# Performance work log

Hardware: AMD Instinct MI355X
Metric: run time of the kernel (lower is better)

## Reference

```python
import jax, jax.numpy as jnp
import numpy as np

B, S, D, H = 2, 2048, 1024, 16  # batch, seq_len, model dim, heads


def setup_inputs() -> dict:
    key = jax.random.key(0)
    ks = jax.random.split(key, 5)
    return {
        "x": jax.random.normal(ks[0], (B, S, D), jnp.float32),
        "idx": jax.random.randint(ks[1], (B,), 0, S),
        "weight": jnp.float32(0.5),
        "attn_forcing": 1,  # static python flag
        "w_qkv": jax.random.normal(ks[2], (D, 3 * D), jnp.float32) * 0.02,
        "b_qkv": jnp.zeros((3 * D,), jnp.float32),
        "w_proj": jax.random.normal(ks[3], (D, D), jnp.float32) * 0.02,
        "b_proj": jnp.zeros((D,), jnp.float32),
    }


def reference(x, idx, weight, attn_forcing, w_qkv, b_qkv, w_proj, b_proj):
    Bx, Sx, Dm = x.shape
    dh = Dm // H
    # qkv projection (Conv1D: x @ w + b)
    qkv = x @ w_qkv + b_qkv  # [B,S,3D]
    q, k, v = jnp.split(qkv, 3, axis=-1)
    q = q.reshape(Bx, Sx, H, dh).transpose(0, 2, 1, 3)  # [B,H,S,dh]
    k = k.reshape(Bx, Sx, H, dh).transpose(0, 2, 1, 3)
    v = v.reshape(Bx, Sx, H, dh).transpose(0, 2, 1, 3)
    alen = jnp.arange(Sx)
    mask = (alen[None, :] <= alen[:, None]).astype(x.dtype)  # [S,S] causal
    w = jnp.einsum('bhqd,bhkd->bhqk', q, k) / jnp.asarray(np.sqrt(dh), x.dtype)
    w = w * mask + jnp.asarray(-1e9, x.dtype) * (1 - mask)
    w = jax.nn.softmax(w, axis=-1)
    if attn_forcing:
        # post-softmax forcing reweight: positions >= idx scaled by weight, then renorm
        a = jnp.where(alen[None, :] >= idx[:, None], weight, jnp.asarray(1.0, x.dtype))  # [B,S]
        w = w * a[:, None, None, :]
        w = w / jnp.sum(w, axis=-1, keepdims=True)
    out = jnp.einsum('bhqk,bhkd->bhqd', w, v)  # [B,H,S,dh]
    out = out.transpose(0, 2, 1, 3).reshape(Bx, Sx, Dm)  # merge heads
    return out @ w_proj + b_proj
```

## Files before the change

### kernel.cpp

```cpp
#include <hip/hip_runtime.h>


typedef __attribute__((ext_vector_type(8))) short short8;
typedef __attribute__((ext_vector_type(4))) float f32x4;

#define MFMA_B16(a, b, c) __builtin_amdgcn_mfma_f32_16x16x32_bf16(a, b, c, 0, 0, 0)

#if __has_builtin(__builtin_amdgcn_exp2f)
#define EXP2(x) __builtin_amdgcn_exp2f(x)
#else
#define EXP2(x) exp2f(x)
#endif

static __device__ __forceinline__ unsigned short f2bf(float f) {
    union { float f; unsigned int u; } v;
    v.f = f;
    unsigned int r = (v.u + 0x7fffu + ((v.u >> 16) & 1u)) >> 16;
    return (unsigned short)r;
}

static __device__ __forceinline__ unsigned int pk_bf16(float a, float b) {
#if __has_builtin(__builtin_amdgcn_cvt_pk_bf16_f32)
    typedef __bf16 bf2 __attribute__((ext_vector_type(2)));
    union { bf2 v; unsigned int u; } c;
    c.v = __builtin_amdgcn_cvt_pk_bf16_f32(a, b);
    return c.u;
#else
    return (unsigned int)f2bf(a) | ((unsigned int)f2bf(b) << 16);
#endif
}

static __device__ __forceinline__ void gl_lds16(const void* g, void* l) {
    __builtin_amdgcn_global_load_lds(
        (const __attribute__((address_space(1))) unsigned int*)g,
        (__attribute__((address_space(3))) unsigned int*)l, 16, 0, 0);
}

__global__ __launch_bounds__(256) void prep_kernel(const float4* __restrict__ x,
                                                   ushort4* __restrict__ xb,
                                                   const float* __restrict__ wqkv,
                                                   unsigned short* __restrict__ wqkvT,
                                                   const float* __restrict__ wproj,
                                                   unsigned short* __restrict__ wprojT) {
    const int bid = blockIdx.x;
    if (bid < 4096) {
        int i = bid * 256 + threadIdx.x;
        float4 v = x[i];
        ushort4 o;
        o.x = f2bf(v.x); o.y = f2bf(v.y); o.z = f2bf(v.z); o.w = f2bf(v.w);
        xb[i] = o;
        return;
    }
    __shared__ float t[32][33];
    const float* in;
    unsigned short* out;
    int R, C, bx, by;
    if (bid < 4096 + 3072) {
        int g = bid - 4096;
        in = wqkv; out = wqkvT; R = 1024; C = 3072;
        bx = g % 96; by = g / 96;
    } else {
        int g = bid - 7168;
        in = wproj; out = wprojT; R = 1024; C = 1024;
        bx = g & 31; by = g >> 5;
    }
    const int c0 = bx * 32, r0 = by * 32;
    const int xx = threadIdx.x & 31, yy0 = threadIdx.x >> 5;
    #pragma unroll
    for (int yy = yy0; yy < 32; yy += 8)
        t[yy][xx] = in[(size_t)(r0 + yy) * C + (c0 + xx)];
    __syncthreads();
    #pragma unroll
    for (int yy = yy0; yy < 32; yy += 8)
        out[(size_t)(c0 + yy) * R + (r0 + xx)] = f2bf(t[xx][yy]);
}

__global__ __launch_bounds__(256) void gemm_qkv_kernel(const unsigned short* __restrict__ A,
                                                       const unsigned short* __restrict__ Bt,
                                                       const float* __restrict__ bias,
                                                       unsigned short* __restrict__ q,
                                                       unsigned short* __restrict__ k,
                                                       unsigned short* __restrict__ vT) {
    __shared__ unsigned short As[128 * 64];
    __shared__ unsigned short Bs[128 * 64];
    const int tid = threadIdx.x;
    const int lane = tid & 63, wave = tid >> 6;
    const int l15 = lane & 15, quad = lane >> 4;
    const int wm = wave >> 1, wn = wave & 1;
    const int row0 = blockIdx.y * 128, col0 = blockIdx.x * 128;
    const int K = 1024;
    const bool isV = (blockIdx.x >= 16);

    int srow[4], scol[4], sdst[4];
    #pragma unroll
    for (int h = 0; h < 4; ++h) {
        int D = h * 256 + wave * 64 + lane;
        srow[h] = D >> 3;
        scol[h] = ((D & 7) ^ (srow[h] & 7)) * 8;
        sdst[h] = (h * 256 + wave * 64) * 8;
    }

    f32x4 acc[4][4] = {};

    for (int kt = 0; kt < K; kt += 64) {
        #pragma unroll
        for (int h = 0; h < 4; ++h) {
            gl_lds16(&A[(size_t)(row0 + srow[h]) * K + kt + scol[h]], &As[sdst[h]]);
            gl_lds16(&Bt[(size_t)(col0 + srow[h]) * K + kt + scol[h]], &Bs[sdst[h]]);
        }
        __syncthreads();
        #pragma unroll
        for (int kk = 0; kk < 2; ++kk) {
            short8 af[4], bf[4];
            #pragma unroll
            for (int i = 0; i < 4; ++i) {
                int r = wm * 64 + i * 16 + l15;
                af[i] = *(const short8*)&As[r * 64 + (((kk * 4 + quad) ^ (r & 7)) * 8)];
            }
            #pragma unroll
            for (int j = 0; j < 4; ++j) {
                int r = wn * 64 + j * 16 + l15;
                bf[j] = *(const short8*)&Bs[r * 64 + (((kk * 4 + quad) ^ (r & 7)) * 8)];
            }
            if (isV) {
                #pragma unroll
                for (int i = 0; i < 4; ++i)
                    #pragma unroll
                    for (int j = 0; j < 4; ++j)
                        acc[i][j] = MFMA_B16(af[i], bf[j], acc[i][j]);
            } else {
                #pragma unroll
                for (int i = 0; i < 4; ++i)
                    #pragma unroll
                    for (int j = 0; j < 4; ++j)
                        acc[i][j] = MFMA_B16(bf[j], af[i], acc[i][j]);
            }
        }
        __syncthreads();
    }

    const int b = row0 >> 11;
    const int s0 = row0 & 2047;
    const float* bb = bias + col0 + wn * 64;

    if (!isV) {
        const int which = blockIdx.x >> 3;
        unsigned short* dst = which ? k : q;
        const float scale = which ? 1.0f : 0.1803368867f;
        const int hh = ((blockIdx.x & 7) << 1) + wn;
        #pragma unroll
        for (int i = 0; i < 4; ++i) {
            const int s = s0 + wm * 64 + i * 16 + l15;
            unsigned short* drow = dst + ((size_t)((b * 16 + hh) * 2048 + s)) * 64;
            #pragma unroll
            for (int j = 0; j < 4; ++j) {
                float4 b4 = ((const float4*)bb)[j * 4 + quad];
                uint2 pv;
                pv.x = pk_bf16((acc[i][j][0] + b4.x) * scale, (acc[i][j][1] + b4.y) * scale);
                pv.y = pk_bf16((acc[i][j][2] + b4.z) * scale, (acc[i][j][3] + b4.w) * scale);
                *(uint2*)&drow[j * 16 + quad * 4] = pv;
            }
        }
    } else {
        const int hh = ((blockIdx.x - 16) << 1) + wn;
        #pragma unroll
        for (int j = 0; j < 4; ++j) {
            const int d = j * 16 + l15;
            const float bv = bb[d];
            unsigned short* drow = vT + ((size_t)((b * 16 + hh) * 64 + d)) * 2048 + s0;
            #pragma unroll
            for (int i = 0; i < 4; ++i) {
                uint2 pv;
                pv.x = pk_bf16(acc[i][j][0] + bv, acc[i][j][1] + bv);
                pv.y = pk_bf16(acc[i][j][2] + bv, acc[i][j][3] + bv);
                *(uint2*)&drow[wm * 64 + i * 16 + quad * 4] = pv;
            }
        }
    }
}

__global__ __launch_bounds__(256) void gemm_proj_kernel(const unsigned short* __restrict__ A,
                                                        const unsigned short* __restrict__ Bt,
                                                        const float* __restrict__ bias,
                                                        float* __restrict__ out) {
    __shared__ unsigned short As[128 * 64];
    __shared__ unsigned short Bs[64 * 64];
    const int tid = threadIdx.x;
    const int lane = tid & 63, wave = tid >> 6;
    const int l15 = lane & 15, quad = lane >> 4;
    const int wm = wave >> 1, wn = wave & 1;
    const int row0 = blockIdx.y * 128, col0 = blockIdx.x * 64;
    const int K = 1024;

    int srow[4], scol[4], sdst[4];
    #pragma unroll
    for (int h = 0; h < 4; ++h) {
        int D = h * 256 + wave * 64 + lane;
        srow[h] = D >> 3;
        scol[h] = ((D & 7) ^ (srow[h] & 7)) * 8;
        sdst[h] = (h * 256 + wave * 64) * 8;
    }

    f32x4 acc[4][2] = {};

    for (int kt = 0; kt < K; kt += 64) {
        #pragma unroll
        for (int h = 0; h < 4; ++h)
            gl_lds16(&A[(size_t)(row0 + srow[h]) * K + kt + scol[h]], &As[sdst[h]]);
        #pragma unroll
        for (int h = 0; h < 2; ++h)
            gl_lds16(&Bt[(size_t)(col0 + srow[h]) * K + kt + scol[h]], &Bs[sdst[h]]);
        __syncthreads();
        #pragma unroll
        for (int kk = 0; kk < 2; ++kk) {
            short8 af[4], bf[2];
            #pragma unroll
            for (int i = 0; i < 4; ++i) {
                int r = wm * 64 + i * 16 + l15;
                af[i] = *(const short8*)&As[r * 64 + (((kk * 4 + quad) ^ (r & 7)) * 8)];
            }
            #pragma unroll
            for (int j = 0; j < 2; ++j) {
                int r = wn * 32 + j * 16 + l15;
                bf[j] = *(const short8*)&Bs[r * 64 + (((kk * 4 + quad) ^ (r & 7)) * 8)];
            }
            #pragma unroll
            for (int i = 0; i < 4; ++i)
                #pragma unroll
                for (int j = 0; j < 2; ++j)
                    acc[i][j] = MFMA_B16(bf[j], af[i], acc[i][j]);
        }
        __syncthreads();
    }

    const float* bb = bias + col0 + wn * 32;
    #pragma unroll
    for (int i = 0; i < 4; ++i) {
        const int row = row0 + wm * 64 + i * 16 + l15;
        #pragma unroll
        for (int j = 0; j < 2; ++j) {
            float4 b4 = ((const float4*)bb)[j * 4 + quad];
            float4 ov;
            ov.x = acc[i][j][0] + b4.x;
            ov.y = acc[i][j][1] + b4.y;
            ov.z = acc[i][j][2] + b4.z;
            ov.w = acc[i][j][3] + b4.w;
            *(float4*)&out[(size_t)row * 1024 + col0 + wn * 32 + j * 16 + quad * 4] = ov;
        }
    }
}

__global__ __launch_bounds__(256) void attn_kernel(const unsigned short* __restrict__ Q,
                                                   const unsigned short* __restrict__ Kg,
                                                   const unsigned short* __restrict__ Vt,
                                                   const int* __restrict__ idx,
                                                   const float* __restrict__ weight,
                                                   const int* __restrict__ forcing,
                                                   unsigned short* __restrict__ O) {
    __shared__ unsigned short Ks[2][4096];
    __shared__ unsigned short Vs[2][4096];
    __shared__ unsigned short Pw[4][1024];

    const int tid = threadIdx.x;
    const int lane = tid & 63, wave = tid >> 6;
    const int l15 = lane & 15, quad = lane >> 4;
    const int bid = blockIdx.x;
    const int u = bid >> 5, a = u & 7, qg = u >> 3;
    const int t = (qg == 0) ? (31 - a) : (qg == 1) ? (16 + a) : (qg == 2) ? (15 - a) : a;
    const int bh = bid & 31;
    const int b = bh >> 4, hh = bh & 15;
    const unsigned short* Qb = Q + (size_t)bh * 2048 * 64;
    const unsigned short* Kh = Kg + (size_t)bh * 2048 * 64;
    const unsigned short* Vh = Vt + (size_t)bh * 2048 * 64;

    const int idxb = idx[b];
    const float lw = (forcing[0] != 0) ? __log2f(weight[0]) : 0.0f;

    const int L0 = wave * 128 + lane;
    const int rS = L0 >> 3;
    const int cS = (L0 & 7) ^ (rS & 7);
    const int ldsOffJ0 = (wave * 128) * 8;
    const int ldsOffJ1 = (wave * 128 + 64) * 8;

    const int q0 = t * 64 + wave * 16;
    const int qrow = q0 + l15;

    short8 aq0 = *(const short8*)&Qb[(q0 + l15) * 64 + quad * 8];
    short8 aq1 = *(const short8*)&Qb[(q0 + l15) * 64 + 32 + quad * 8];

    const short8 ones8 = {0x3F80, 0x3F80, 0x3F80, 0x3F80, 0x3F80, 0x3F80, 0x3F80, 0x3F80};

    f32x4 o[4] = {};
    f32x4 lsum = {};

    const int nkb = t + 1;

    {
        const unsigned short* kg = Kh + (size_t)rS * 64 + cS * 8;
        const unsigned short* vg = Vh + (size_t)rS * 2048 + cS * 8;
        gl_lds16(kg,            &Ks[0][ldsOffJ0]);
        gl_lds16(kg + 8 * 64,   &Ks[0][ldsOffJ1]);
        gl_lds16(vg,            &Vs[0][ldsOffJ0]);
        gl_lds16(vg + 8 * 2048, &Vs[0][ldsOffJ1]);
    }
    __syncthreads();

    unsigned short* const pwb = &Pw[wave][0];
    const int pwr = l15 * 64;
    const int pa7 = l15 & 7;

    for (int kb = 0; kb < nkb; ++kb) {
        const int cur = kb & 1;
        const int kbase = kb * 64;
        if (kb + 1 < nkb) {
            const int nb = kbase + 64;
            const unsigned short* kg = Kh + (size_t)(nb + rS) * 64 + cS * 8;
            const unsigned short* vg = Vh + (size_t)rS * 2048 + nb + cS * 8;
            gl_lds16(kg,            &Ks[cur ^ 1][ldsOffJ0]);
            gl_lds16(kg + 8 * 64,   &Ks[cur ^ 1][ldsOffJ1]);
            gl_lds16(vg,            &Vs[cur ^ 1][ldsOffJ0]);
            gl_lds16(vg + 8 * 2048, &Vs[cur ^ 1][ldsOffJ1]);
        }

        const bool fullF = (kbase >= idxb);
        const bool bndF = (!fullF) && (kbase + 63 >= idxb);
        const float zu = fullF ? lw : 0.0f;

        f32x4 sT[4];
        #pragma unroll
        for (int kt = 0; kt < 4; ++kt) {
            const int row = kt * 16 + l15;
            short8 k0 = *(const short8*)&Ks[cur][row * 64 + ((quad ^ (row & 7)) * 8)];
            short8 k1 = *(const short8*)&Ks[cur][row * 64 + (((4 + quad) ^ (row & 7)) * 8)];
            f32x4 z;
            if (!bndF) {
                z[0] = zu; z[1] = zu; z[2] = zu; z[3] = zu;
            } else {
                #pragma unroll
                for (int r = 0; r < 4; ++r)
                    z[r] = (kbase + kt * 16 + quad * 4 + r >= idxb) ? lw : 0.0f;
            }
            z = MFMA_B16(k0, aq0, z);
            z = MFMA_B16(k1, aq1, z);
            sT[kt] = z;
        }

        if (kb == t) {
            #pragma unroll
            for (int kt = 0; kt < 4; ++kt)
                #pragma unroll
                for (int r = 0; r < 4; ++r)
                    if (kbase + kt * 16 + quad * 4 + r > qrow) sT[kt][r] = -3.0e38f;
        }

        #pragma unroll
        for (int kt = 0; kt < 4; ++kt)
            #pragma unroll
            for (int r = 0; r < 4; ++r)
                sT[kt][r] = EXP2(sT[kt][r]);

        #pragma unroll
        for (int kt = 0; kt < 4; ++kt) {
            unsigned int* pw = (unsigned int*)&pwb[pwr +
                (((kt * 2 + (quad >> 1)) ^ pa7) * 8) + (quad & 1) * 4];
            pw[0] = pk_bf16(sT[kt][0], sT[kt][1]);
            pw[1] = pk_bf16(sT[kt][2], sT[kt][3]);
        }

        short8 bp0 = *(const short8*)&pwb[pwr + ((quad ^ pa7) * 8)];
        short8 bp1 = *(const short8*)&pwb[pwr + (((4 + quad) ^ pa7) * 8)];

        lsum = MFMA_B16(ones8, bp0, lsum);
        lsum = MFMA_B16(ones8, bp1, lsum);

        #pragma unroll
        for (int dt = 0; dt < 4; ++dt) {
            const int row = dt * 16 + l15;
            short8 vf0 = *(const short8*)&Vs[cur][row * 64 + ((quad ^ (row & 7)) * 8)];
            short8 vf1 = *(const short8*)&Vs[cur][row * 64 + (((4 + quad) ^ (row & 7)) * 8)];
            f32x4 oo = o[dt];
            oo = MFMA_B16(vf0, bp0, oo);
            oo = MFMA_B16(vf1, bp1, oo);
            o[dt] = oo;
        }

        __syncthreads();
    }

    const float inv = 1.0f / lsum[0];
    unsigned short* sc = &Ks[0][0] + wave * 1152;
    #pragma unroll
    for (int dt = 0; dt < 4; ++dt)
        #pragma unroll
        for (int r = 0; r < 4; ++r)
            sc[l15 * 72 + dt * 16 + quad * 4 + r] = f2bf(o[dt][r] * inv);
    const size_t rowoff = ((size_t)(b * 2048 + q0 + l15)) * 1024 + hh * 64;
    #pragma unroll
    for (int h = 0; h < 2; ++h) {
        short8 v8 = *(const short8*)&sc[l15 * 72 + quad * 16 + h * 8];
        *(short8*)&O[rowoff + quad * 16 + h * 8] = v8;
    }
}

extern "C" void kernel_launch(void* const* d_in, const int* in_sizes, int n_in,
                              void* d_out, int out_size, void* d_ws, size_t ws_size,
                              hipStream_t stream) {
    const float* x        = (const float*)d_in[0];
    const int*   idx      = (const int*)d_in[1];
    const float* weight   = (const float*)d_in[2];
    const int*   forcing  = (const int*)d_in[3];
    const float* w_qkv    = (const float*)d_in[4];
    const float* b_qkv    = (const float*)d_in[5];
    const float* w_proj   = (const float*)d_in[6];
    const float* b_proj   = (const float*)d_in[7];
    float* out = (float*)d_out;

    char* ws = (char*)d_ws;
    unsigned short* xb      = (unsigned short*)(ws);
    unsigned short* wqkvT   = (unsigned short*)(ws + 8388608);
    unsigned short* wprojT  = (unsigned short*)(ws + 14680064);
    unsigned short* qbuf    = (unsigned short*)(ws + 16777216);
    unsigned short* kbuf    = (unsigned short*)(ws + 25165824);
    unsigned short* vTbuf   = (unsigned short*)(ws + 33554432);
    unsigned short* attn_out = xb;

    prep_kernel<<<8192, 256, 0, stream>>>((const float4*)x, (ushort4*)xb,
                                          w_qkv, wqkvT, w_proj, wprojT);
    gemm_qkv_kernel<<<dim3(24, 32), 256, 0, stream>>>(xb, wqkvT, b_qkv, qbuf, kbuf, vTbuf);
    attn_kernel<<<1024, 256, 0, stream>>>(qbuf, kbuf, vTbuf, idx, weight, forcing, attn_out);
    gemm_proj_kernel<<<dim3(16, 32), 256, 0, stream>>>(attn_out, wprojT, b_proj, out);
}
```

Baseline: 189.4 us.

## Process two query tiles per attention block to reuse staged K/V

Each attention workgroup now handles 128 query rows (two 64-row tiles, A and B) instead of 64. Every K/V tile loaded into LDS therefore feeds both tiles, roughly halving global K/V traffic and the number of blocks launched. Tile A skips its last key block on the diagonal. The grid shrinks from 1024 to 512 blocks, the balanced t-ordering is replaced by a simple descending order, and register and LDS use per block increase. This risks lower occupancy and worse load balance across CUs.

```diff
diff --git a/kernel.cpp b/kernel.cpp
--- a/kernel.cpp
+++ b/kernel.cpp
@@ -259,14 +259,13 @@
                                                    unsigned short* __restrict__ O) {
     __shared__ unsigned short Ks[2][4096];
     __shared__ unsigned short Vs[2][4096];
-    __shared__ unsigned short Pw[4][1024];
+    __shared__ unsigned short Pw[4][2048];
 
     const int tid = threadIdx.x;
     const int lane = tid & 63, wave = tid >> 6;
     const int l15 = lane & 15, quad = lane >> 4;
     const int bid = blockIdx.x;
-    const int u = bid >> 5, a = u & 7, qg = u >> 3;
-    const int t = (qg == 0) ? (31 - a) : (qg == 1) ? (16 + a) : (qg == 2) ? (15 - a) : a;
+    const int t = 15 - (bid >> 5);
     const int bh = bid & 31;
     const int b = bh >> 4, hh = bh & 15;
     const unsigned short* Qb = Q + (size_t)bh * 2048 * 64;
@@ -282,18 +281,21 @@
     const int ldsOffJ0 = (wave * 128) * 8;
     const int ldsOffJ1 = (wave * 128 + 64) * 8;
 
-    const int q0 = t * 64 + wave * 16;
-    const int qrow = q0 + l15;
-
-    short8 aq0 = *(const short8*)&Qb[(q0 + l15) * 64 + quad * 8];
-    short8 aq1 = *(const short8*)&Qb[(q0 + l15) * 64 + 32 + quad * 8];
+    const int q0 = t * 128 + wave * 16;
+    const int qrowA = q0 + l15;
+    const int qrowB = q0 + 64 + l15;
+
+    short8 aqA0 = *(const short8*)&Qb[(q0 + l15) * 64 + quad * 8];
+    short8 aqA1 = *(const short8*)&Qb[(q0 + l15) * 64 + 32 + quad * 8];
+    short8 aqB0 = *(const short8*)&Qb[(q0 + 64 + l15) * 64 + quad * 8];
+    short8 aqB1 = *(const short8*)&Qb[(q0 + 64 + l15) * 64 + 32 + quad * 8];
 
     const short8 ones8 = {0x3F80, 0x3F80, 0x3F80, 0x3F80, 0x3F80, 0x3F80, 0x3F80, 0x3F80};
 
-    f32x4 o[4] = {};
-    f32x4 lsum = {};
-
-    const int nkb = t + 1;
+    f32x4 oA[4] = {}, oB[4] = {};
+    f32x4 lsA = {}, lsB = {};
+
+    const int nkb = 2 * t + 2;
 
     {
         const unsigned short* kg = Kh + (size_t)rS * 64 + cS * 8;
@@ -322,83 +324,139 @@
             gl_lds16(vg + 8 * 2048, &Vs[cur ^ 1][ldsOffJ1]);
         }
 
+        const bool liveA = (kb + 1 < nkb);
+        const bool diagA = (kb + 2 == nkb);
+        const bool diagB = (kb + 1 == nkb);
+
         const bool fullF = (kbase >= idxb);
         const bool bndF = (!fullF) && (kbase + 63 >= idxb);
         const float zu = fullF ? lw : 0.0f;
-
-        f32x4 sT[4];
+        f32x4 zi[4];
+        #pragma unroll
+        for (int kt = 0; kt < 4; ++kt) {
+            if (!bndF) {
+                zi[kt][0] = zu; zi[kt][1] = zu; zi[kt][2] = zu; zi[kt][3] = zu;
+            } else {
+                #pragma unroll
+                for (int r = 0; r < 4; ++r)
+                    zi[kt][r] = (kbase + kt * 16 + quad * 4 + r >= idxb) ? lw : 0.0f;
+            }
+        }
+
+        f32x4 sA[4], sB[4];
         #pragma unroll
         for (int kt = 0; kt < 4; ++kt) {
             const int row = kt * 16 + l15;
             short8 k0 = *(const short8*)&Ks[cur][row * 64 + ((quad ^ (row & 7)) * 8)];
             short8 k1 = *(const short8*)&Ks[cur][row * 64 + (((4 + quad) ^ (row & 7)) * 8)];
-            f32x4 z;
-            if (!bndF) {
-                z[0] = zu; z[1] = zu; z[2] = zu; z[3] = zu;
-            } else {
+            if (liveA) {
+                f32x4 z = zi[kt];
+                z = MFMA_B16(k0, aqA0, z);
+                z = MFMA_B16(k1, aqA1, z);
+                sA[kt] = z;
+            }
+            f32x4 z = zi[kt];
+            z = MFMA_B16(k0, aqB0, z);
+            z = MFMA_B16(k1, aqB1, z);
+            sB[kt] = z;
+        }
+
+        if (diagA) {
+            #pragma unroll
+            for (int kt = 0; kt < 4; ++kt)
                 #pragma unroll
                 for (int r = 0; r < 4; ++r)
-                    z[r] = (kbase + kt * 16 + quad * 4 + r >= idxb) ? lw : 0.0f;
-            }
-            z = MFMA_B16(k0, aq0, z);
-            z = MFMA_B16(k1, aq1, z);
-            sT[kt] = z;
-        }
-
-        if (kb == t) {
+                    if (kbase + kt * 16 + quad * 4 + r > qrowA) sA[kt][r] = -3.0e38f;
+        }
+        if (diagB) {
             #pragma unroll
             for (int kt = 0; kt < 4; ++kt)
                 #pragma unroll
                 for (int r = 0; r < 4; ++r)
-                    if (kbase + kt * 16 + quad * 4 + r > qrow) sT[kt][r] = -3.0e38f;
-        }
-
-        #pragma unroll
-        for (int kt = 0; kt < 4; ++kt)
-            #pragma unroll
-            for (int r = 0; r < 4; ++r)
-                sT[kt][r] = EXP2(sT[kt][r]);
-
+                    if (kbase + kt * 16 + quad * 4 + r > qrowB) sB[kt][r] = -3.0e38f;
+        }
+
+        if (liveA) {
+            #pragma unroll
+            for (int kt = 0; kt < 4; ++kt) {
+                #pragma unroll
+                for (int r = 0; r < 4; ++r) sA[kt][r] = EXP2(sA[kt][r]);
+                unsigned int* pw = (unsigned int*)&pwb[pwr +
+                    (((kt * 2 + (quad >> 1)) ^ pa7) * 8) + (quad & 1) * 4];
+                pw[0] = pk_bf16(sA[kt][0], sA[kt][1]);
+                pw[1] = pk_bf16(sA[kt][2], sA[kt][3]);
+            }
+        }
         #pragma unroll
         for (int kt = 0; kt < 4; ++kt) {
-            unsigned int* pw = (unsigned int*)&pwb[pwr +
+            #pragma unroll
+            for (int r = 0; r < 4; ++r) sB[kt][r] = EXP2(sB[kt][r]);
+            unsigned int* pw = (unsigned int*)&pwb[1024 + pwr +
                 (((kt * 2 + (quad >> 1)) ^ pa7) * 8) + (quad & 1) * 4];
-            pw[0] = pk_bf16(sT[kt][0], sT[kt][1]);
-            pw[1] = pk_bf16(sT[kt][2], sT[kt][3]);
-        }
-
-        short8 bp0 = *(const short8*)&pwb[pwr + ((quad ^ pa7) * 8)];
-        short8 bp1 = *(const short8*)&pwb[pwr + (((4 + quad) ^ pa7) * 8)];
-
-        lsum = MFMA_B16(ones8, bp0, lsum);
-        lsum = MFMA_B16(ones8, bp1, lsum);
+            pw[0] = pk_bf16(sB[kt][0], sB[kt][1]);
+            pw[1] = pk_bf16(sB[kt][2], sB[kt][3]);
+        }
+
+        short8 bpA0, bpA1;
+        if (liveA) {
+            bpA0 = *(const short8*)&pwb[pwr + ((quad ^ pa7) * 8)];
+            bpA1 = *(const short8*)&pwb[pwr + (((4 + quad) ^ pa7) * 8)];
+            lsA = MFMA_B16(ones8, bpA0, lsA);
+            lsA = MFMA_B16(ones8, bpA1, lsA);
+        }
+        short8 bpB0 = *(const short8*)&pwb[1024 + pwr + ((quad ^ pa7) * 8)];
+        short8 bpB1 = *(const short8*)&pwb[1024 + pwr + (((4 + quad) ^ pa7) * 8)];
+        lsB = MFMA_B16(ones8, bpB0, lsB);
+        lsB = MFMA_B16(ones8, bpB1, lsB);
 
         #pragma unroll
         for (int dt = 0; dt < 4; ++dt) {
             const int row = dt * 16 + l15;
             short8 vf0 = *(const short8*)&Vs[cur][row * 64 + ((quad ^ (row & 7)) * 8)];
             short8 vf1 = *(const short8*)&Vs[cur][row * 64 + (((4 + quad) ^ (row & 7)) * 8)];
-            f32x4 oo = o[dt];
-            oo = MFMA_B16(vf0, bp0, oo);
-            oo = MFMA_B16(vf1, bp1, oo);
-            o[dt] = oo;
+            if (liveA) {
+                f32x4 oo = oA[dt];
+                oo = MFMA_B16(vf0, bpA0, oo);
+                oo = MFMA_B16(vf1, bpA1, oo);
+                oA[dt] = oo;
+            }
+            f32x4 oo = oB[dt];
+            oo = MFMA_B16(vf0, bpB0, oo);
+            oo = MFMA_B16(vf1, bpB1, oo);
+            oB[dt] = oo;
         }
 
         __syncthreads();
     }
 
-    const float inv = 1.0f / lsum[0];
     unsigned short* sc = &Ks[0][0] + wave * 1152;
-    #pragma unroll
-    for (int dt = 0; dt < 4; ++dt)
-        #pragma unroll
-        for (int r = 0; r < 4; ++r)
-            sc[l15 * 72 + dt * 16 + quad * 4 + r] = f2bf(o[dt][r] * inv);
-    const size_t rowoff = ((size_t)(b * 2048 + q0 + l15)) * 1024 + hh * 64;
-    #pragma unroll
-    for (int h = 0; h < 2; ++h) {
-        short8 v8 = *(const short8*)&sc[l15 * 72 + quad * 16 + h * 8];
-        *(short8*)&O[rowoff + quad * 16 + h * 8] = v8;
+    {
+        const float inv = 1.0f / lsA[0];
+        #pragma unroll
+        for (int dt = 0; dt < 4; ++dt)
+            #pragma unroll
+            for (int r = 0; r < 4; ++r)
+                sc[l15 * 72 + dt * 16 + quad * 4 + r] = f2bf(oA[dt][r] * inv);
+        const size_t rowoff = ((size_t)(b * 2048 + q0 + l15)) * 1024 + hh * 64;
+        #pragma unroll
+        for (int h = 0; h < 2; ++h) {
+            short8 v8 = *(const short8*)&sc[l15 * 72 + quad * 16 + h * 8];
+            *(short8*)&O[rowoff + quad * 16 + h * 8] = v8;
+        }
+    }
+    {
+        const float inv = 1.0f / lsB[0];
+        #pragma unroll
+        for (int dt = 0; dt < 4; ++dt)
+            #pragma unroll
+            for (int r = 0; r < 4; ++r)
+                sc[l15 * 72 + dt * 16 + quad * 4 + r] = f2bf(oB[dt][r] * inv);
+        const size_t rowoff = ((size_t)(b * 2048 + q0 + 64 + l15)) * 1024 + hh * 64;
+        #pragma unroll
+        for (int h = 0; h < 2; ++h) {
+            short8 v8 = *(const short8*)&sc[l15 * 72 + quad * 16 + h * 8];
+            *(short8*)&O[rowoff + quad * 16 + h * 8] = v8;
+        }
     }
 }
 
@@ -427,6 +485,6 @@
     prep_kernel<<<8192, 256, 0, stream>>>((const float4*)x, (ushort4*)xb,
                                           w_qkv, wqkvT, w_proj, wprojT);
     gemm_qkv_kernel<<<dim3(24, 32), 256, 0, stream>>>(xb, wqkvT, b_qkv, qbuf, kbuf, vTbuf);
-    attn_kernel<<<1024, 256, 0, stream>>>(qbuf, kbuf, vTbuf, idx, weight, forcing, attn_out);
+    attn_kernel<<<512, 256, 0, stream>>>(qbuf, kbuf, vTbuf, idx, weight, forcing, attn_out);
     gemm_proj_kernel<<<dim3(16, 32), 256, 0, stream>>>(attn_out, wprojT, b_proj, out);
 }
```

New measurement: 209.4 us. +10.6%, slower.
